# Kernel optimization log

Measured on AMD Instinct MI355X. Metric: run time of the kernel, lower is better.

Reference implementation:

```python
import jax, jax.numpy as jnp
import numpy as np

SEQ_LEN = 512
JOINT_DIM = 96
DECAY = 0.8


def _predefined_weights(n: int, decay: float) -> np.ndarray:
    # W[i, j] = decay**(i-j) for j <= i, each row normalized to sum 1.
    i = np.arange(n)[:, None]
    j = np.arange(n)[None, :]
    lower = j <= i
    exponent = np.where(lower, i - j, 0)
    w = np.where(lower, decay ** exponent.astype(np.float64), 0.0)
    row_sum = w.sum(axis=1, keepdims=True)
    w = np.where(row_sum > 0, w / row_sum, w)
    return w.astype(np.float32)


def setup_inputs() -> dict:
    key = jax.random.key(0)
    kx, ko = jax.random.split(key)
    x = jax.random.normal(kx, (64, SEQ_LEN, JOINT_DIM), dtype=jnp.float32)
    # learnable parameter (initialized to zeros in the module; small noise for generality)
    learnable_offset = 0.02 * jax.random.normal(ko, (JOINT_DIM, SEQ_LEN, SEQ_LEN), dtype=jnp.float32)
    predefined_weights = jnp.asarray(_predefined_weights(SEQ_LEN, DECAY))
    return {"x": x, "learnable_offset": learnable_offset, "predefined_weights": predefined_weights}


def reference(x, learnable_offset, predefined_weights):
    # masks[j] = softmax(predefined + offset[j], axis=-1)   -> [J, N, N]
    masks = jax.nn.softmax(predefined_weights[None, :, :] + learnable_offset, axis=-1)
    # out[b, n, j] = sum_m masks[j, n, m] * x[b, m, j]      -> [B, N, J]
    return jnp.einsum('jnm,bmj->bnj', masks, x)
```

## Files before the change

kernel.cpp:

```cpp
#include <hip/hip_runtime.h>

#define BATCH 64
#define SEQ   512
#define JDIM  96
#define TN    64

typedef __attribute__((ext_vector_type(8))) short bf16x8;
typedef __attribute__((ext_vector_type(4))) float f32x4;

__device__ __forceinline__ unsigned short f2bf(float f) {
  unsigned u = __float_as_uint(f);
  u += 0x7FFFu + ((u >> 16) & 1u);
  return (unsigned short)(u >> 16);
}

__global__ __launch_bounds__(256) void transpose_in_kernel(
    const float* __restrict__ x, unsigned short* __restrict__ xT) {
  __shared__ float tile[JDIM * 65];
  const int r0 = blockIdx.x * 64;
  const int R = BATCH * SEQ;
  for (int idx = threadIdx.x; idx < 64 * 24; idx += 256) {
    int rr = idx / 24, jg = idx - rr * 24;
    float4 v = *(const float4*)(x + (size_t)(r0 + rr) * JDIM + 4 * jg);
    tile[(4 * jg + 0) * 65 + rr] = v.x;
    tile[(4 * jg + 1) * 65 + rr] = v.y;
    tile[(4 * jg + 2) * 65 + rr] = v.z;
    tile[(4 * jg + 3) * 65 + rr] = v.w;
  }
  __syncthreads();
  for (int idx = threadIdx.x; idx < JDIM * 8; idx += 256) {
    int jj = idx >> 3, rg = idx & 7;
    const float* t = &tile[jj * 65 + 8 * rg];
    uint4 pk;
    pk.x = (unsigned)f2bf(t[0]) | ((unsigned)f2bf(t[1]) << 16);
    pk.y = (unsigned)f2bf(t[2]) | ((unsigned)f2bf(t[3]) << 16);
    pk.z = (unsigned)f2bf(t[4]) | ((unsigned)f2bf(t[5]) << 16);
    pk.w = (unsigned)f2bf(t[6]) | ((unsigned)f2bf(t[7]) << 16);
    *(uint4*)(&xT[(size_t)jj * R + r0 + 8 * rg]) = pk;
  }
}

__global__ __launch_bounds__(256) void fused_kernel(
    const unsigned short* __restrict__ xT,
    const float* __restrict__ off,
    const float* __restrict__ pre,
    float* __restrict__ outT) {
  const int j  = blockIdx.x % JDIM;
  const int n0 = (blockIdx.x / JDIM) * TN;

  const int tid  = threadIdx.x;
  const int lane = tid & 63;
  const int wid  = tid >> 6;
  const int ln   = lane & 15;
  const int quad = lane >> 4;
  const int nrow = n0 + 16 * wid + ln;

  const unsigned short* xTj = xT + (size_t)j * (BATCH * SEQ);
  const float* pO = off + (size_t)j * (SEQ * SEQ) + (size_t)nrow * SEQ + 8 * quad;
  const float* pP = pre + (size_t)nrow * SEQ + 8 * quad;
  const unsigned short* pA = xTj + (size_t)ln * SEQ + 8 * quad;

  f32x4 acc[4];
#pragma unroll
  for (int i = 0; i < 4; ++i) acc[i] = (f32x4){0.f, 0.f, 0.f, 0.f};
  float Lsum = 0.f;

#pragma unroll
  for (int ks = 0; ks < SEQ; ks += 32) {
    const float4 o0 = *(const float4*)(pO + ks);
    const float4 o1 = *(const float4*)(pO + ks + 4);
    const float4 p0 = *(const float4*)(pP + ks);
    const float4 p1 = *(const float4*)(pP + ks + 4);
    bf16x8 af[4];
#pragma unroll
    for (int i = 0; i < 4; ++i)
      af[i] = *(const bf16x8*)(pA + (size_t)(16 * i) * SEQ + ks);

    const float e0 = __expf(o0.x + p0.x);
    const float e1 = __expf(o0.y + p0.y);
    const float e2 = __expf(o0.z + p0.z);
    const float e3 = __expf(o0.w + p0.w);
    const float e4 = __expf(o1.x + p1.x);
    const float e5 = __expf(o1.y + p1.y);
    const float e6 = __expf(o1.z + p1.z);
    const float e7 = __expf(o1.w + p1.w);
    Lsum += ((e0 + e1) + (e2 + e3)) + ((e4 + e5) + (e6 + e7));

    union { uint4 u; bf16x8 v; } bp;
    bp.u.x = (unsigned)f2bf(e0) | ((unsigned)f2bf(e1) << 16);
    bp.u.y = (unsigned)f2bf(e2) | ((unsigned)f2bf(e3) << 16);
    bp.u.z = (unsigned)f2bf(e4) | ((unsigned)f2bf(e5) << 16);
    bp.u.w = (unsigned)f2bf(e6) | ((unsigned)f2bf(e7) << 16);

#pragma unroll
    for (int i = 0; i < 4; ++i)
      acc[i] = __builtin_amdgcn_mfma_f32_16x16x32_bf16(af[i], bp.v, acc[i], 0, 0, 0);
  }

  Lsum += __shfl_xor(Lsum, 16, 64);
  Lsum += __shfl_xor(Lsum, 32, 64);
  const float linv = 1.0f / Lsum;

  float* outTj = outT + (size_t)j * (SEQ * BATCH);
#pragma unroll
  for (int i = 0; i < 4; ++i) {
    float4 v;
    v.x = acc[i][0] * linv;
    v.y = acc[i][1] * linv;
    v.z = acc[i][2] * linv;
    v.w = acc[i][3] * linv;
    *(float4*)(&outTj[(size_t)nrow * BATCH + 16 * i + 4 * quad]) = v;
  }
}

__global__ __launch_bounds__(256) void transpose_out_kernel(
    const float* __restrict__ outT, float* __restrict__ out) {
  __shared__ float tile[JDIM * 65];
  const int n = blockIdx.x;
  for (int idx = threadIdx.x; idx < JDIM * 16; idx += 256) {
    int jj = idx >> 4, g = idx & 15;
    float4 v = *(const float4*)(outT + ((size_t)jj * SEQ + n) * BATCH + 4 * g);
    float* t = &tile[jj * 65 + 4 * g];
    t[0] = v.x; t[1] = v.y; t[2] = v.z; t[3] = v.w;
  }
  __syncthreads();
  for (int idx = threadIdx.x; idx < BATCH * 24; idx += 256) {
    int b = idx / 24, jg = idx - b * 24;
    float4 w;
    w.x = tile[(4 * jg + 0) * 65 + b];
    w.y = tile[(4 * jg + 1) * 65 + b];
    w.z = tile[(4 * jg + 2) * 65 + b];
    w.w = tile[(4 * jg + 3) * 65 + b];
    *(float4*)(out + ((size_t)b * SEQ + n) * JDIM + 4 * jg) = w;
  }
}

extern "C" void kernel_launch(void* const* d_in, const int* in_sizes, int n_in,
                              void* d_out, int out_size, void* d_ws, size_t ws_size,
                              hipStream_t stream) {
  const float* x   = (const float*)d_in[0];
  const float* off = (const float*)d_in[1];
  const float* pre = (const float*)d_in[2];
  float* out = (float*)d_out;

  unsigned short* xT = (unsigned short*)d_ws;
  float* outT = (float*)((char*)d_ws + (size_t)JDIM * BATCH * SEQ * sizeof(unsigned short));

  transpose_in_kernel<<<BATCH * SEQ / 64, 256, 0, stream>>>(x, xT);
  fused_kernel<<<JDIM * (SEQ / TN), 256, 0, stream>>>(xT, off, pre, outT);
  transpose_out_kernel<<<SEQ, 256, 0, stream>>>(outT, out);
}
```

Baseline: 189.5 us.

## Split K across warps in fused kernel with shared-memory reduction

Each block now handles 16 rows of n for one joint, and its four warps each cover a quarter of the K=512 dimension. Partial accumulators and row sums are reduced through shared memory before the normalized output is written. This raises the block count fourfold and shortens each warp's serial load/MFMA chain, exposing more memory-level parallelism for streaming the large offset tensor. The cost is an extra shared-memory reduction and barrier per block. Each block also re-reads the full xT slice for its joint, so total x traffic rises, though it should mostly hit in cache.

```diff
diff --git a/kernel.cpp b/kernel.cpp
--- a/kernel.cpp
+++ b/kernel.cpp
@@ -3,7 +3,7 @@
 #define BATCH 64
 #define SEQ   512
 #define JDIM  96
-#define TN    64
+#define TNS   16
 
 typedef __attribute__((ext_vector_type(8))) short bf16x8;
 typedef __attribute__((ext_vector_type(4))) float f32x4;
@@ -40,25 +40,29 @@
   }
 }
 
-__global__ __launch_bounds__(256) void fused_kernel(
+__global__ __launch_bounds__(256, 6) void fused_kernel(
     const unsigned short* __restrict__ xT,
     const float* __restrict__ off,
     const float* __restrict__ pre,
     float* __restrict__ outT) {
-  const int j  = blockIdx.x % JDIM;
-  const int n0 = (blockIdx.x / JDIM) * TN;
+  __shared__ float accs[4 * 4 * 16 * 17];
+  __shared__ float Lw[4][16];
 
-  const int tid  = threadIdx.x;
-  const int lane = tid & 63;
-  const int wid  = tid >> 6;
-  const int ln   = lane & 15;
-  const int quad = lane >> 4;
-  const int nrow = n0 + 16 * wid + ln;
+  const int j  = blockIdx.x >> 5;
+  const int n0 = (blockIdx.x & 31) * TNS;
+
+  const int tid   = threadIdx.x;
+  const int lane  = tid & 63;
+  const int wid   = tid >> 6;
+  const int ln    = lane & 15;
+  const int quad  = lane >> 4;
+  const int nrow  = n0 + ln;
+  const int kbase = 128 * wid;
 
   const unsigned short* xTj = xT + (size_t)j * (BATCH * SEQ);
-  const float* pO = off + (size_t)j * (SEQ * SEQ) + (size_t)nrow * SEQ + 8 * quad;
-  const float* pP = pre + (size_t)nrow * SEQ + 8 * quad;
-  const unsigned short* pA = xTj + (size_t)ln * SEQ + 8 * quad;
+  const float* pO = off + (size_t)j * (SEQ * SEQ) + (size_t)nrow * SEQ + kbase + 8 * quad;
+  const float* pP = pre + (size_t)nrow * SEQ + kbase + 8 * quad;
+  const unsigned short* pA = xTj + (size_t)ln * SEQ + kbase + 8 * quad;
 
   f32x4 acc[4];
 #pragma unroll
@@ -66,7 +70,7 @@
   float Lsum = 0.f;
 
 #pragma unroll
-  for (int ks = 0; ks < SEQ; ks += 32) {
+  for (int ks = 0; ks < 128; ks += 32) {
     const float4 o0 = *(const float4*)(pO + ks);
     const float4 o1 = *(const float4*)(pO + ks + 4);
     const float4 p0 = *(const float4*)(pP + ks);
@@ -99,18 +103,32 @@
 
   Lsum += __shfl_xor(Lsum, 16, 64);
   Lsum += __shfl_xor(Lsum, 32, 64);
-  const float linv = 1.0f / Lsum;
+  if (quad == 0) Lw[wid][ln] = Lsum;
 
+#pragma unroll
+  for (int i = 0; i < 4; ++i)
+#pragma unroll
+    for (int r = 0; r < 4; ++r)
+      accs[((wid * 4 + i) * 16 + 4 * quad + r) * 17 + ln] = acc[i][r];
+  __syncthreads();
+
+  const int n  = tid >> 4;
+  const int bg = tid & 15;
+  const int ii = bg >> 2;
+  const int qq = bg & 3;
+  const float linv = 1.0f / (((Lw[0][n] + Lw[1][n]) + (Lw[2][n] + Lw[3][n])));
+  float4 v;
+  float* vp = &v.x;
+#pragma unroll
+  for (int r = 0; r < 4; ++r) {
+    float s = 0.f;
+#pragma unroll
+    for (int w = 0; w < 4; ++w)
+      s += accs[((w * 4 + ii) * 16 + 4 * qq + r) * 17 + n];
+    vp[r] = s * linv;
+  }
   float* outTj = outT + (size_t)j * (SEQ * BATCH);
-#pragma unroll
-  for (int i = 0; i < 4; ++i) {
-    float4 v;
-    v.x = acc[i][0] * linv;
-    v.y = acc[i][1] * linv;
-    v.z = acc[i][2] * linv;
-    v.w = acc[i][3] * linv;
-    *(float4*)(&outTj[(size_t)nrow * BATCH + 16 * i + 4 * quad]) = v;
-  }
+  *(float4*)(&outTj[(size_t)(n0 + n) * BATCH + 4 * bg]) = v;
 }
 
 __global__ __launch_bounds__(256) void transpose_out_kernel(
@@ -147,6 +165,6 @@
   float* outT = (float*)((char*)d_ws + (size_t)JDIM * BATCH * SEQ * sizeof(unsigned short));
 
   transpose_in_kernel<<<BATCH * SEQ / 64, 256, 0, stream>>>(x, xT);
-  fused_kernel<<<JDIM * (SEQ / TN), 256, 0, stream>>>(xT, off, pre, outT);
+  fused_kernel<<<JDIM * (SEQ / TNS), 256, 0, stream>>>(xT, off, pre, outT);
   transpose_out_kernel<<<SEQ, 256, 0, stream>>>(outT, out);
 }
```

Result: slower. 194.3 us (+2.5%).
